# Performance work log

Hardware: AMD Instinct MI355X
Metric: run time of the kernel (lower is better)

## Reference

```python
import jax, jax.numpy as jnp
import numpy as np
import math

D, H, DK, DFF, B, T, K = 512, 8, 64, 2048, 8, 512, 31
P = 2 * T - 1  # rel-pos length


def _ln(x, g, b, eps=1e-5):
    mu = jnp.mean(x, -1, keepdims=True)
    var = jnp.var(x, -1, keepdims=True)
    return (x - mu) * jax.lax.rsqrt(var + eps) * g + b


def _silu(x):
    return x * jax.nn.sigmoid(x)


def _rel_shift(x):
    # x: [B,H,T,P] -> NeMo-style relative shift
    b, h, t, p = x.shape
    x = jnp.pad(x, ((0, 0), (0, 0), (0, 0), (1, 0)))
    x = x.reshape(b, h, p + 1, t)
    return x[:, :, 1:, :].reshape(b, h, t, p)


def _forward(x, pos_emb, ln1_g, ln1_b, ff1_w1, ff1_b1, ff1_w2, ff1_b2,
             lna_g, lna_b, wq, bq, wk, bk, wv, bv, wo, bo, wpos, pbu, pbv,
             lnc_g, lnc_b, pw1_w, pw1_b, dw_w, dw_b, cln_g, cln_b, pw2_w, pw2_b,
             ln2_g, ln2_b, ff2_w1, ff2_b1, ff2_w2, ff2_b2, lno_g, lno_b):
    b, t, d = x.shape
    h, dk = pbu.shape
    # FF1 (half-step residual)
    r = x
    y = _ln(x, ln1_g, ln1_b)
    y = _silu(y @ ff1_w1 + ff1_b1) @ ff1_w2 + ff1_b2
    r = r + 0.5 * y
    # Rel-pos multi-head attention
    y = _ln(r, lna_g, lna_b)
    q = (y @ wq + bq).reshape(b, t, h, dk)
    k = (y @ wk + bk).reshape(b, t, h, dk)
    v = (y @ wv + bv).reshape(b, t, h, dk)
    p = (pos_emb @ wpos).reshape(pos_emb.shape[0], -1, h, dk)[0]  # [P,H,dk]
    ac = jnp.einsum('bthd,bshd->bhts', q + pbu, k)
    bd = jnp.einsum('bthd,phd->bhtp', q + pbv, p)
    bd = _rel_shift(bd)[..., :t]
    attn = jax.nn.softmax((ac + bd) / math.sqrt(dk), axis=-1)
    o = jnp.einsum('bhts,bshd->bthd', attn, v).reshape(b, t, d) @ wo + bo
    r = r + o
    # Conformer convolution module (layer_norm variant)
    y = _ln(r, lnc_g, lnc_b)
    y = y @ pw1_w + pw1_b                       # [B,T,2D] pointwise conv1
    a, g = jnp.split(y, 2, axis=-1)
    y = a * jax.nn.sigmoid(g)                   # GLU over channels
    y = jnp.transpose(y, (0, 2, 1))             # [B,D,T]
    pad = (dw_w.shape[1] - 1) // 2
    y = jax.lax.conv_general_dilated(
        y, dw_w[:, None, :], (1,), [(pad, pad)],
        feature_group_count=d, dimension_numbers=('NCH', 'OIH', 'NCH'))
    y = y + dw_b[None, :, None]
    y = jnp.transpose(y, (0, 2, 1))             # [B,T,D]
    y = _ln(y, cln_g, cln_b)
    y = _silu(y) @ pw2_w + pw2_b                # pointwise conv2
    r = r + y
    # FF2 (half-step residual)
    y = _ln(r, ln2_g, ln2_b)
    y = _silu(y @ ff2_w1 + ff2_b1) @ ff2_w2 + ff2_b2
    r = r + 0.5 * y
    return _ln(r, lno_g, lno_b)


def setup_inputs() -> dict:
    key = jax.random.key(0)
    ks = iter(jax.random.split(key, 64))
    rn = lambda shape, s=0.05: jax.random.normal(next(ks), shape, dtype=jnp.float32) * s
    ones = lambda n: jnp.ones((n,), jnp.float32)
    zeros = lambda n: jnp.zeros((n,), jnp.float32)
    return dict(
        x=jax.random.normal(next(ks), (B, T, D), jnp.float32),
        pos_emb=jax.random.normal(next(ks), (1, P, D), jnp.float32),
        ln1_g=ones(D), ln1_b=zeros(D),
        ff1_w1=rn((D, DFF)), ff1_b1=zeros(DFF), ff1_w2=rn((DFF, D)), ff1_b2=zeros(D),
        lna_g=ones(D), lna_b=zeros(D),
        wq=rn((D, D)), bq=zeros(D), wk=rn((D, D)), bk=zeros(D),
        wv=rn((D, D)), bv=zeros(D), wo=rn((D, D)), bo=zeros(D),
        wpos=rn((D, D)), pbu=rn((H, DK)), pbv=rn((H, DK)),
        lnc_g=ones(D), lnc_b=zeros(D),
        pw1_w=rn((D, 2 * D)), pw1_b=zeros(2 * D),
        dw_w=rn((D, K)), dw_b=zeros(D),
        cln_g=ones(D), cln_b=zeros(D),
        pw2_w=rn((D, D)), pw2_b=zeros(D),
        ln2_g=ones(D), ln2_b=zeros(D),
        ff2_w1=rn((D, DFF)), ff2_b1=zeros(DFF), ff2_w2=rn((DFF, D)), ff2_b2=zeros(D),
        lno_g=ones(D), lno_b=zeros(D))


def reference(x, pos_emb, ln1_g, ln1_b, ff1_w1, ff1_b1, ff1_w2, ff1_b2,
              lna_g, lna_b, wq, bq, wk, bk, wv, bv, wo, bo, wpos, pbu, pbv,
              lnc_g, lnc_b, pw1_w, pw1_b, dw_w, dw_b, cln_g, cln_b, pw2_w, pw2_b,
              ln2_g, ln2_b, ff2_w1, ff2_b1, ff2_w2, ff2_b2, lno_g, lno_b):
    return _forward(x, pos_emb, ln1_g, ln1_b, ff1_w1, ff1_b1, ff1_w2, ff1_b2,
                    lna_g, lna_b, wq, bq, wk, bk, wv, bv, wo, bo, wpos, pbu, pbv,
                    lnc_g, lnc_b, pw1_w, pw1_b, dw_w, dw_b, cln_g, cln_b, pw2_w, pw2_b,
                    ln2_g, ln2_b, ff2_w1, ff2_b1, ff2_w2, ff2_b2, lno_g, lno_b)
```

## Files before the change

### kernel.cpp

```cpp
#include <hip/hip_runtime.h>
#include <hip/hip_bf16.h>

#define Bb 8
#define Tt 512
#define Dd 512
#define Hh 8
#define DKk 64
#define DFFf 2048
#define Pp 1023
#define KCc 31
#define BTt 4096
#define QS 1536

typedef __hip_bfloat16 bf16;
typedef __attribute__((ext_vector_type(8))) short short8;
typedef __attribute__((ext_vector_type(4))) short s4v;
typedef __attribute__((ext_vector_type(4))) float f32x4;

union BFU { __hip_bfloat16 h; short s; };
static __device__ __forceinline__ short bfbits(float f) {
    BFU u; u.h = __float2bfloat16(f); return u.s;
}
static __device__ __forceinline__ float bff(short s) {
    BFU u; u.s = s; return __bfloat162float(u.h);
}
static __device__ __forceinline__ unsigned pk2(float a, float b) {
    return (unsigned)(unsigned short)bfbits(a) | ((unsigned)(unsigned short)bfbits(b) << 16);
}

static __device__ __forceinline__ int dflag(const void* lg) {
    return ((const unsigned*)lg)[0] == 0x3F803F80u;
}

#define GLD16(g, l) __builtin_amdgcn_global_load_lds(                          \
    (const __attribute__((address_space(1))) void*)(g),                        \
    (__attribute__((address_space(3))) void*)(l), 16, 0, 0)

struct CvtDesc { const void* src; unsigned n; unsigned off; unsigned startBlk; };
struct CvtArgs { CvtDesc d[32]; };

__global__ __launch_bounds__(256) void cvt_batch_k(CvtArgs args, int ncv,
                                                   bf16* __restrict__ dst,
                                                   const void* __restrict__ lg) {
    int bid = blockIdx.x;
    int ti = 0;
    while (ti + 1 < ncv && bid >= (int)args.d[ti + 1].startBlk) ti++;
    CvtDesc de = args.d[ti];
    unsigned i = (bid - de.startBlk) * 256u + threadIdx.x;
    if (i >= de.n) return;
    float v;
    if (dflag(lg)) v = __bfloat162float(((const bf16*)de.src)[i]);
    else           v = ((const float*)de.src)[i];
    dst[de.off + i] = __float2bfloat16(v);
}

struct TD { const void* src; unsigned doff, R, C, startBlk; };
struct TArgs { TD d[11]; };

__global__ __launch_bounds__(256) void transpose_batch_k(TArgs ta, bf16* __restrict__ wt,
                                                         const void* __restrict__ lg) {
    int bid = blockIdx.x;
    int ti = 0;
    while (ti + 1 < 11 && bid >= (int)ta.d[ti + 1].startBlk) ti++;
    TD t = ta.d[ti];
    int tile = bid - t.startBlk;
    int ntc = t.C >> 5;
    int tr = tile / ntc, tc = tile % ntc;
    __shared__ short tl[32][33];
    short* out = (short*)wt + t.doff;
    int tx = threadIdx.x & 31, ty = threadIdx.x >> 5;
    int fl = dflag(lg);
#pragma unroll
    for (int i = 0; i < 32; i += 8) {
        size_t idx = (size_t)(tr * 32 + ty + i) * t.C + tc * 32 + tx;
        short v;
        if (fl) v = ((const short*)t.src)[idx];
        else    v = bfbits(((const float*)t.src)[idx]);
        tl[ty + i][tx] = v;
    }
    __syncthreads();
#pragma unroll
    for (int i = 0; i < 32; i += 8)
        out[(size_t)(tc * 32 + ty + i) * t.R + tr * 32 + tx] = tl[tx][ty + i];
}

__global__ __launch_bounds__(256) void prep_misc_k(const void* __restrict__ dww, bf16* __restrict__ dwT,
                                                   const void* __restrict__ bq, const void* __restrict__ bk,
                                                   const void* __restrict__ bv, bf16* __restrict__ bqkv,
                                                   const void* __restrict__ lg) {
    int i = blockIdx.x * 256 + threadIdx.x;
    int fl = dflag(lg);
    if (i < Dd * KCc) {
        int d = i / KCc, j = i % KCc;
        short v = fl ? ((const short*)dww)[i] : bfbits(((const float*)dww)[i]);
        ((short*)dwT)[j * Dd + d] = v;
    } else {
        int j = i - Dd * KCc;
        if (j < QS) {
            const void* s = (j < 512) ? bq : ((j < 1024) ? bk : bv);
            int idx = j & 511;
            short v = fl ? ((const short*)s)[idx] : bfbits(((const float*)s)[idx]);
            ((short*)bqkv)[j] = v;
        }
    }
}

template <int SILU>
__global__ __launch_bounds__(256) void ln_k(const float* __restrict__ in,
                                            const bf16* __restrict__ g,
                                            const bf16* __restrict__ b,
                                            bf16* __restrict__ out) {
    int row = blockIdx.x;
    int tid = threadIdx.x;
    float2 v = ((const float2*)(in + (size_t)row * Dd))[tid];
    float s = v.x + v.y;
    float ss = v.x * v.x + v.y * v.y;
#pragma unroll
    for (int off = 32; off > 0; off >>= 1) {
        s += __shfl_xor(s, off);
        ss += __shfl_xor(ss, off);
    }
    __shared__ float red[2][4];
    int wid = tid >> 6;
    if ((tid & 63) == 0) { red[0][wid] = s; red[1][wid] = ss; }
    __syncthreads();
    float S = red[0][0] + red[0][1] + red[0][2] + red[0][3];
    float SS = red[1][0] + red[1][1] + red[1][2] + red[1][3];
    float mean = S * (1.0f / Dd);
    float var = SS * (1.0f / Dd) - mean * mean;
    float rstd = rsqrtf(var + 1e-5f);
    unsigned gp = *(const unsigned*)((const short*)g + 2 * tid);
    unsigned bp = *(const unsigned*)((const short*)b + 2 * tid);
    float o0 = (v.x - mean) * rstd * bff((short)(gp & 0xFFFF)) + bff((short)(bp & 0xFFFF));
    float o1 = (v.y - mean) * rstd * bff((short)(gp >> 16)) + bff((short)(bp >> 16));
    if (SILU) {
        o0 = o0 / (1.0f + __expf(-o0));
        o1 = o1 / (1.0f + __expf(-o1));
    }
    *(unsigned*)((short*)out + (size_t)row * Dd + 2 * tid) = pk2(o0, o1);
}

__global__ __launch_bounds__(256) void ln_x_k(const void* __restrict__ x,
                                              const bf16* __restrict__ g,
                                              const bf16* __restrict__ b,
                                              float* __restrict__ r,
                                              bf16* __restrict__ out,
                                              const void* __restrict__ lg) {
    int row = blockIdx.x;
    int tid = threadIdx.x;
    size_t base = (size_t)row * Dd;
    float v0, v1;
    if (dflag(lg)) {
        unsigned xp = *(const unsigned*)((const short*)x + base + 2 * tid);
        v0 = bff((short)(xp & 0xFFFF));
        v1 = bff((short)(xp >> 16));
    } else {
        float2 xv = ((const float2*)((const float*)x + base))[tid];
        v0 = xv.x; v1 = xv.y;
    }
    ((float2*)(r + base))[tid] = make_float2(v0, v1);
    float s = v0 + v1;
    float ss = v0 * v0 + v1 * v1;
#pragma unroll
    for (int off = 32; off > 0; off >>= 1) {
        s += __shfl_xor(s, off);
        ss += __shfl_xor(ss, off);
    }
    __shared__ float red[2][4];
    int wid = tid >> 6;
    if ((tid & 63) == 0) { red[0][wid] = s; red[1][wid] = ss; }
    __syncthreads();
    float S = red[0][0] + red[0][1] + red[0][2] + red[0][3];
    float SS = red[1][0] + red[1][1] + red[1][2] + red[1][3];
    float mean = S * (1.0f / Dd);
    float var = SS * (1.0f / Dd) - mean * mean;
    float rstd = rsqrtf(var + 1e-5f);
    unsigned gp = *(const unsigned*)((const short*)g + 2 * tid);
    unsigned bp = *(const unsigned*)((const short*)b + 2 * tid);
    float o0 = (v0 - mean) * rstd * bff((short)(gp & 0xFFFF)) + bff((short)(bp & 0xFFFF));
    float o1 = (v1 - mean) * rstd * bff((short)(gp >> 16)) + bff((short)(bp >> 16));
    *(unsigned*)((short*)out + base + 2 * tid) = pk2(o0, o1);
}

__global__ __launch_bounds__(256) void ln_out_k(const float* __restrict__ in,
                                                const bf16* __restrict__ g,
                                                const bf16* __restrict__ b,
                                                void* __restrict__ out,
                                                const void* __restrict__ lg) {
    int row = blockIdx.x;
    int tid = threadIdx.x;
    size_t base = (size_t)row * Dd;
    float2 v = ((const float2*)(in + base))[tid];
    float s = v.x + v.y;
    float ss = v.x * v.x + v.y * v.y;
#pragma unroll
    for (int off = 32; off > 0; off >>= 1) {
        s += __shfl_xor(s, off);
        ss += __shfl_xor(ss, off);
    }
    __shared__ float red[2][4];
    int wid = tid >> 6;
    if ((tid & 63) == 0) { red[0][wid] = s; red[1][wid] = ss; }
    __syncthreads();
    float S = red[0][0] + red[0][1] + red[0][2] + red[0][3];
    float SS = red[1][0] + red[1][1] + red[1][2] + red[1][3];
    float mean = S * (1.0f / Dd);
    float var = SS * (1.0f / Dd) - mean * mean;
    float rstd = rsqrtf(var + 1e-5f);
    unsigned gp = *(const unsigned*)((const short*)g + 2 * tid);
    unsigned bp = *(const unsigned*)((const short*)b + 2 * tid);
    float o0 = (v.x - mean) * rstd * bff((short)(gp & 0xFFFF)) + bff((short)(bp & 0xFFFF));
    float o1 = (v.y - mean) * rstd * bff((short)(gp >> 16)) + bff((short)(bp >> 16));
    if (dflag(lg)) {
        *(unsigned*)((short*)out + base + 2 * tid) = pk2(o0, o1);
    } else {
        ((float2*)((float*)out + base))[tid] = make_float2(o0, o1);
    }
}

template <int BM, int BN, int BK, int WM, int WN, typename CT, int ACT, int RES, int VT>
__global__ __launch_bounds__(256) void gemm_mfma_k(const bf16* __restrict__ Abf,
                                                   const bf16* __restrict__ WT,
                                                   const bf16* __restrict__ bias,
                                                   const float* __restrict__ resid,
                                                   CT* __restrict__ C,
                                                   bf16* __restrict__ vt,
                                                   int M, int N, int Kd, float alpha) {
    constexpr int MT = WM / 16, NT = WN / 16;
    constexpr int WX = BN / WN;
    constexpr int CPB = BK / 8;
    constexpr int KS = BK / 32;
    __shared__ __align__(16) short As[BM * BK];
    __shared__ __align__(16) short Bs[BN * BK];
    int tid = threadIdx.x;
    int wid = tid >> 6, lane = tid & 63;
    int lm = lane & 15, quad = lane >> 4;
    int wy = wid / WX, wx = wid % WX;
    int bm = blockIdx.y * BM, bn = blockIdx.x * BN;
    const short* Ag = (const short*)Abf;
    const short* Bg = (const short*)WT;

    f32x4 acc[MT][NT] = {};

    for (int k0 = 0; k0 < Kd; k0 += BK) {
#pragma unroll
        for (int it = 0; it < BM * CPB / 256; it++) {
            int c = it * 256 + tid;
            int row = c / CPB;
            int q = (c % CPB) ^ (row & 7);
            int gr = bm + row;
            if (gr > M - 1) gr = M - 1;
            GLD16(Ag + (size_t)gr * Kd + k0 + q * 8, As + (it * 256 + wid * 64) * 8);
        }
#pragma unroll
        for (int it = 0; it < BN * CPB / 256; it++) {
            int c = it * 256 + tid;
            int row = c / CPB;
            int q = (c % CPB) ^ (row & 7);
            GLD16(Bg + (size_t)(bn + row) * Kd + k0 + q * 8, Bs + (it * 256 + wid * 64) * 8);
        }
        __syncthreads();
        short8 af[MT][KS], bfv[NT][KS];
#pragma unroll
        for (int mt = 0; mt < MT; mt++) {
            int row = wy * WM + mt * 16 + lm;
#pragma unroll
            for (int ks = 0; ks < KS; ks++)
                af[mt][ks] = *(const short8*)&As[row * BK + (((ks * 4 + quad) ^ (row & 7)) * 8)];
        }
#pragma unroll
        for (int nt = 0; nt < NT; nt++) {
            int row = wx * WN + nt * 16 + lm;
#pragma unroll
            for (int ks = 0; ks < KS; ks++)
                bfv[nt][ks] = *(const short8*)&Bs[row * BK + (((ks * 4 + quad) ^ (row & 7)) * 8)];
        }
#pragma unroll
        for (int ks = 0; ks < KS; ks++)
#pragma unroll
            for (int mt = 0; mt < MT; mt++)
#pragma unroll
                for (int nt = 0; nt < NT; nt++)
                    acc[mt][nt] = __builtin_amdgcn_mfma_f32_16x16x32_bf16(af[mt][ks], bfv[nt][ks], acc[mt][nt], 0, 0, 0);
        __syncthreads();
    }

#pragma unroll
    for (int mt = 0; mt < MT; mt++) {
#pragma unroll
        for (int nt = 0; nt < NT; nt++) {
            int gcol = bn + wx * WN + nt * 16 + lm;
            int growb = bm + wy * WM + mt * 16 + quad * 4;
            if (VT && gcol >= 1024) {
                float bi = bias ? __bfloat162float(bias[gcol]) : 0.f;
                s4v pk;
#pragma unroll
                for (int r = 0; r < 4; r++) pk[r] = bfbits(acc[mt][nt][r] + bi);
                *(s4v*)((short*)vt + (size_t)((growb >> 9) * 512 + (gcol - 1024)) * 512 + (growb & 511)) = pk;
            } else {
#pragma unroll
                for (int r = 0; r < 4; r++) {
                    int grow = growb + r;
                    if (grow >= M) continue;
                    float v = acc[mt][nt][r];
                    if (bias) v += __bfloat162float(bias[gcol]);
                    if (ACT == 1) v = v / (1.0f + __expf(-v));
                    if (RES == 1) v = resid[(size_t)grow * N + gcol] + alpha * v;
                    C[(size_t)grow * N + gcol] = (CT)v;
                }
            }
        }
    }
}

__global__ __launch_bounds__(256) void gemm_glu_k(const bf16* __restrict__ Abf,
                                                  const bf16* __restrict__ WT,
                                                  const bf16* __restrict__ bias,
                                                  bf16* __restrict__ C) {
    constexpr int BM = 64, BN = 64, BK = 64, WM = 32, WN = 32;
    constexpr int MT = WM / 16, NT = WN / 16, WX = BN / WN, CPB = BK / 8, KS = BK / 32;
    __shared__ __align__(16) short As[BM * BK];
    __shared__ __align__(16) short Bs[2 * BN * BK];
    int tid = threadIdx.x;
    int wid = tid >> 6, lane = tid & 63;
    int lm = lane & 15, quad = lane >> 4;
    int wy = wid / WX, wx = wid % WX;
    int bm = blockIdx.y * BM, bn = blockIdx.x * BN;
    const short* Ag = (const short*)Abf;
    const short* Bg = (const short*)WT;

    f32x4 acc[MT][NT][2] = {};

    for (int k0 = 0; k0 < Dd; k0 += BK) {
#pragma unroll
        for (int it = 0; it < BM * CPB / 256; it++) {
            int c = it * 256 + tid;
            int row = c / CPB;
            int q = (c % CPB) ^ (row & 7);
            GLD16(Ag + (size_t)(bm + row) * Dd + k0 + q * 8, As + (it * 256 + wid * 64) * 8);
        }
#pragma unroll
        for (int it = 0; it < 2 * BN * CPB / 256; it++) {
            int c = it * 256 + tid;
            int row = c / CPB;
            int q = (c % CPB) ^ (row & 7);
            int wrow = (row < BN) ? (bn + row) : (512 + bn + row - BN);
            GLD16(Bg + (size_t)wrow * Dd + k0 + q * 8, Bs + (it * 256 + wid * 64) * 8);
        }
        __syncthreads();
        short8 af[MT][KS], bfv[NT][2][KS];
#pragma unroll
        for (int mt = 0; mt < MT; mt++) {
            int row = wy * WM + mt * 16 + lm;
#pragma unroll
            for (int ks = 0; ks < KS; ks++)
                af[mt][ks] = *(const short8*)&As[row * BK + (((ks * 4 + quad) ^ (row & 7)) * 8)];
        }
#pragma unroll
        for (int nt = 0; nt < NT; nt++) {
#pragma unroll
            for (int hf = 0; hf < 2; hf++) {
                int row = hf * BN + wx * WN + nt * 16 + lm;
#pragma unroll
                for (int ks = 0; ks < KS; ks++)
                    bfv[nt][hf][ks] = *(const short8*)&Bs[row * BK + (((ks * 4 + quad) ^ (row & 7)) * 8)];
            }
        }
#pragma unroll
        for (int ks = 0; ks < KS; ks++)
#pragma unroll
            for (int mt = 0; mt < MT; mt++)
#pragma unroll
                for (int nt = 0; nt < NT; nt++) {
                    acc[mt][nt][0] = __builtin_amdgcn_mfma_f32_16x16x32_bf16(af[mt][ks], bfv[nt][0][ks], acc[mt][nt][0], 0, 0, 0);
                    acc[mt][nt][1] = __builtin_amdgcn_mfma_f32_16x16x32_bf16(af[mt][ks], bfv[nt][1][ks], acc[mt][nt][1], 0, 0, 0);
                }
        __syncthreads();
    }

#pragma unroll
    for (int mt = 0; mt < MT; mt++) {
#pragma unroll
        for (int nt = 0; nt < NT; nt++) {
#pragma unroll
            for (int r = 0; r < 4; r++) {
                int grow = bm + wy * WM + mt * 16 + quad * 4 + r;
                int gcol = bn + wx * WN + nt * 16 + lm;
                float va = acc[mt][nt][0][r] + __bfloat162float(bias[gcol]);
                float vg = acc[mt][nt][1][r] + __bfloat162float(bias[512 + gcol]);
                float v = va / (1.0f + __expf(-vg));
                C[(size_t)grow * Dd + gcol] = __float2bfloat16(v);
            }
        }
    }
}

#define SST 516

__global__ __launch_bounds__(256, 4) void attn_mfma_k(const bf16* __restrict__ qkv,
                                                      const bf16* __restrict__ p,
                                                      const bf16* __restrict__ vT,
                                                      const bf16* __restrict__ pbu,
                                                      const bf16* __restrict__ pbv,
                                                      bf16* __restrict__ out) {
    __shared__ float S[16][SST];
    __shared__ float lsum[16];
    short* Pbase = (short*)&S[0][0];
    int tid = threadIdx.x;
    int wid = tid >> 6;
    int lane = tid & 63;
    int lm = lane & 15;
    int quad = lane >> 4;
    int bidx = blockIdx.x;
    int b = bidx >> 8;
    int h = (bidx >> 5) & 7;
    int t0 = (bidx & 31) * 16;

    const short* qkvs = (const short*)qkv;
    const short* ps = (const short*)p;

    short8 qu[2], qv[2];
    {
        size_t rowbase = ((size_t)(b * Tt + t0 + lm) * QS) + h * DKk;
#pragma unroll
        for (int ksp = 0; ksp < 2; ksp++) {
            int kk = ksp * 32 + quad * 8;
            short8 raw = *(const short8*)(qkvs + rowbase + kk);
#pragma unroll
            for (int j = 0; j < 8; j++) {
                float qf = bff(raw[j]);
                qu[ksp][j] = bfbits(qf + __bfloat162float(pbu[h * DKk + kk + j]));
                qv[ksp][j] = bfbits(qf + __bfloat162float(pbv[h * DKk + kk + j]));
            }
        }
    }

    const float scale = 0.125f;

#pragma unroll
    for (int i = 0; i < 8; i++) {
        int st = wid + i * 4;
        f32x4 c = {0.f, 0.f, 0.f, 0.f};
        size_t krow = ((size_t)(b * Tt + st * 16 + lm) * QS) + 512 + h * DKk;
#pragma unroll
        for (int ksp = 0; ksp < 2; ksp++) {
            short8 bf = *(const short8*)(qkvs + krow + ksp * 32 + quad * 8);
            c = __builtin_amdgcn_mfma_f32_16x16x32_bf16(qu[ksp], bf, c, 0, 0, 0);
        }
#pragma unroll
        for (int r = 0; r < 4; r++)
            S[quad * 4 + r][st * 16 + lm] = scale * c[r];
    }
    __syncthreads();

    int win0 = 496 - t0;
#pragma unroll
    for (int i = 0; i < 8; i++) {
        int pt = wid + i * 4;
        f32x4 c = {0.f, 0.f, 0.f, 0.f};
        int prow = win0 + pt * 16 + lm;
        bool ok = (prow < Pp);
        size_t pbase = (size_t)prow * Dd + h * DKk;
#pragma unroll
        for (int ksp = 0; ksp < 2; ksp++) {
            short8 bf;
            if (ok) bf = *(const short8*)(ps + pbase + ksp * 32 + quad * 8);
            else { bf = short8{0,0,0,0,0,0,0,0}; }
            c = __builtin_amdgcn_mfma_f32_16x16x32_bf16(qv[ksp], bf, c, 0, 0, 0);
        }
#pragma unroll
        for (int r = 0; r < 4; r++) {
            int m = quad * 4 + r;
            int s = pt * 16 + lm + m - 15;
            if (s >= 0 && s < Tt) S[m][s] += scale * c[r];
        }
    }
    if (wid == 0) {
        int pt = 32;
        f32x4 c = {0.f, 0.f, 0.f, 0.f};
        int prow = win0 + pt * 16 + lm;
        bool ok = (prow < Pp);
        size_t pbase = (size_t)prow * Dd + h * DKk;
#pragma unroll
        for (int ksp = 0; ksp < 2; ksp++) {
            short8 bf;
            if (ok) bf = *(const short8*)(ps + pbase + ksp * 32 + quad * 8);
            else { bf = short8{0,0,0,0,0,0,0,0}; }
            c = __builtin_amdgcn_mfma_f32_16x16x32_bf16(qv[ksp], bf, c, 0, 0, 0);
        }
#pragma unroll
        for (int r = 0; r < 4; r++) {
            int m = quad * 4 + r;
            int s = pt * 16 + lm + m - 15;
            if (s >= 0 && s < Tt) S[m][s] += scale * c[r];
        }
    }
    __syncthreads();

    {
        int srow = tid >> 4;
        int g2 = (tid & 15) * 2;
        float mx = -1e30f;
#pragma unroll 8
        for (int i = 0; i < 16; i++) {
            mx = fmaxf(mx, fmaxf(S[srow][i * 32 + g2], S[srow][i * 32 + g2 + 1]));
        }
#pragma unroll
        for (int off = 1; off < 16; off <<= 1) mx = fmaxf(mx, __shfl_xor(mx, off));
        float sum = 0.f;
        short* prow = Pbase + (size_t)srow * (SST * 2);
#pragma unroll 8
        for (int i = 0; i < 16; i++) {
            float e0 = __expf(S[srow][i * 32 + g2] - mx);
            float e1 = __expf(S[srow][i * 32 + g2 + 1] - mx);
            sum += e0 + e1;
            *(unsigned*)&prow[i * 32 + g2] = pk2(e0, e1);
        }
#pragma unroll
        for (int off = 1; off < 16; off <<= 1) sum += __shfl_xor(sum, off);
        if (g2 == 0) lsum[srow] = sum;
    }
    __syncthreads();

    int d0 = wid * 16;
    f32x4 o = {0.f, 0.f, 0.f, 0.f};
    const short* vrow = (const short*)vT + ((size_t)(b * Hh + h) * DKk + d0 + lm) * Tt;
    const short* parow = Pbase + (size_t)lm * (SST * 2);
#pragma unroll
    for (int ksp = 0; ksp < 16; ksp++) {
        int kk = ksp * 32 + quad * 8;
        short8 a = *(const short8*)(parow + kk);
        short8 bf = *(const short8*)(vrow + kk);
        o = __builtin_amdgcn_mfma_f32_16x16x32_bf16(a, bf, o, 0, 0, 0);
    }
    short* os = (short*)out;
#pragma unroll
    for (int r = 0; r < 4; r++) {
        int m = quad * 4 + r;
        os[((size_t)(b * Tt + t0 + m) * Dd) + h * DKk + d0 + lm] = bfbits(o[r] / lsum[m]);
    }
}

__global__ __launch_bounds__(256) void dwconv_ln_k(const bf16* __restrict__ in,
                                                   const bf16* __restrict__ wT,
                                                   const bf16* __restrict__ bdw,
                                                   const bf16* __restrict__ g,
                                                   const bf16* __restrict__ bb,
                                                   bf16* __restrict__ out) {
    int row = blockIdx.x * 4 + (threadIdx.x >> 6);
    int lane = threadIdx.x & 63;
    int d0 = lane * 8;
    int t = row & 511, b = row >> 9;
    const short* ins = (const short*)in + (size_t)b * Tt * Dd;
    const short* wts = (const short*)wT;
    float acc[8];
    short8 bv = *(const short8*)((const short*)bdw + d0);
#pragma unroll
    for (int e = 0; e < 8; e++) acc[e] = bff(bv[e]);
#pragma unroll
    for (int j = 0; j < KCc; j++) {
        int tt = t + j - 15;
        if (tt < 0 || tt >= Tt) continue;
        short8 iv = *(const short8*)(ins + (size_t)tt * Dd + d0);
        short8 wv = *(const short8*)(wts + j * Dd + d0);
#pragma unroll
        for (int e = 0; e < 8; e++) acc[e] += bff(iv[e]) * bff(wv[e]);
    }
    float s = 0.f, ss = 0.f;
#pragma unroll
    for (int e = 0; e < 8; e++) { s += acc[e]; ss += acc[e] * acc[e]; }
#pragma unroll
    for (int off = 32; off > 0; off >>= 1) {
        s += __shfl_xor(s, off);
        ss += __shfl_xor(ss, off);
    }
    float mean = s * (1.0f / Dd);
    float var = ss * (1.0f / Dd) - mean * mean;
    float rstd = rsqrtf(var + 1e-5f);
    short8 gv = *(const short8*)((const short*)g + d0);
    short8 bbv = *(const short8*)((const short*)bb + d0);
    short8 ov;
#pragma unroll
    for (int e = 0; e < 8; e++) {
        float o = (acc[e] - mean) * rstd * bff(gv[e]) + bff(bbv[e]);
        o = o / (1.0f + __expf(-o));
        ov[e] = bfbits(o);
    }
    *(short8*)((short*)out + (size_t)row * Dd + d0) = ov;
}

extern "C" void kernel_launch(void* const* d_in, const int* in_sizes, int n_in,
                              void* d_out, int out_size, void* d_ws, size_t ws_size,
                              hipStream_t stream) {
    char* base = (char*)d_ws;
    bf16* wb = (bf16*)(base + 256);

    size_t woff[39];
    size_t acc = 0;
    for (int i = 1; i < 39; i++) { woff[i] = acc; acc += (size_t)in_sizes[i]; }
    size_t wbytes = (2 * acc + 255) & ~(size_t)255;

    const size_t NBT = (size_t)BTt * Dd;
    float* r   = (float*)((char*)wb + wbytes);
    bf16* a    = (bf16*)((char*)r + NBT * 4);
    bf16* big  = a + NBT;
    bf16* pbuf = big + (size_t)BTt * DFFf;
    bf16* wt   = pbuf + (size_t)Pp * Dd;

    const void* lg = d_in[2];

    bf16* c_pos   = wb + woff[1];
    bf16* c_ln1g  = wb + woff[2],  *c_ln1b = wb + woff[3];
    bf16* c_f1b1  = wb + woff[5];
    bf16* c_f1b2  = wb + woff[7];
    bf16* c_lnag  = wb + woff[8],  *c_lnab = wb + woff[9];
    bf16* c_bo    = wb + woff[17];
    bf16* c_pbu   = wb + woff[19], *c_pbv  = wb + woff[20];
    bf16* c_lncg  = wb + woff[21], *c_lncb = wb + woff[22];
    bf16* c_p1b   = wb + woff[24];
    bf16* c_dwb   = wb + woff[26];
    bf16* c_clng  = wb + woff[27], *c_clnb = wb + woff[28];
    bf16* c_p2b   = wb + woff[30];
    bf16* c_ln2g  = wb + woff[31], *c_ln2b = wb + woff[32];
    bf16* c_f2b1  = wb + woff[34];
    bf16* c_f2b2  = wb + woff[36];
    bf16* c_lnog  = wb + woff[37], *c_lnob = wb + woff[38];

    const int tin[11]  = {4, 6, 10, 12, 14, 16, 18, 23, 29, 33, 35};
    const unsigned tR[11] = {512, 2048, 512, 512, 512, 512, 512, 512, 512, 512, 2048};
    const unsigned tC[11] = {2048, 512, 512, 512, 512, 512, 512, 1024, 512, 2048, 512};
    size_t toff[11]; size_t tacc = 0;
    for (int i = 0; i < 11; i++) { toff[i] = tacc; tacc += (size_t)tR[i] * tC[i]; }
    bf16* t_f1w1 = wt + toff[0];
    bf16* t_f1w2 = wt + toff[1];
    bf16* t_wqkv = wt + toff[2];
    bf16* t_wo   = wt + toff[5];
    bf16* t_wpos = wt + toff[6];
    bf16* t_p1w  = wt + toff[7];
    bf16* t_p2w  = wt + toff[8];
    bf16* t_f2w1 = wt + toff[9];
    bf16* t_f2w2 = wt + toff[10];
    bf16* bias_qkv = wt + tacc;
    bf16* dwT      = bias_qkv + QS;
    bf16* vTb      = dwT + KCc * Dd;

    dim3 blk(256);

    bool skip[39] = {};
    for (int i = 0; i < 11; i++) skip[tin[i]] = true;
    skip[11] = skip[13] = skip[15] = skip[25] = true;
    CvtArgs ca;
    int ncv = 0;
    unsigned blkacc = 0;
    for (int i = 1; i < 39; i++) {
        if (skip[i]) continue;
        ca.d[ncv].src = d_in[i];
        ca.d[ncv].n = (unsigned)in_sizes[i];
        ca.d[ncv].off = (unsigned)woff[i];
        ca.d[ncv].startBlk = blkacc;
        blkacc += (unsigned)((in_sizes[i] + 255) / 256);
        ncv++;
    }
    cvt_batch_k<<<blkacc, blk, 0, stream>>>(ca, ncv, wb, lg);

    TArgs ta;
    unsigned tblk = 0;
    for (int i = 0; i < 11; i++) {
        ta.d[i].src = d_in[tin[i]];
        ta.d[i].doff = (unsigned)toff[i];
        ta.d[i].R = tR[i];
        ta.d[i].C = tC[i];
        ta.d[i].startBlk = tblk;
        tblk += (tR[i] >> 5) * (tC[i] >> 5);
    }
    transpose_batch_k<<<tblk, blk, 0, stream>>>(ta, wt, lg);
    prep_misc_k<<<(Dd * KCc + QS + 255) / 256, blk, 0, stream>>>(
        d_in[25], dwT, d_in[11], d_in[13], d_in[15], bias_qkv, lg);

    auto g128 = [](int M, int N) { return dim3(N / 128, M / 128); };
    auto g64  = [](int M, int N) { return dim3(N / 64, (M + 63) / 64); };

    ln_x_k<<<BTt, blk, 0, stream>>>(d_in[0], c_ln1g, c_ln1b, r, a, lg);
    gemm_mfma_k<128, 128, 64, 64, 64, bf16, 1, 0, 0><<<g128(BTt, DFFf), blk, 0, stream>>>(
        a, t_f1w1, c_f1b1, nullptr, big, nullptr, BTt, DFFf, Dd, 0.f);
    gemm_mfma_k<64, 64, 128, 32, 32, float, 0, 1, 0><<<g64(BTt, Dd), blk, 0, stream>>>(
        big, t_f1w2, c_f1b2, r, r, nullptr, BTt, Dd, DFFf, 0.5f);

    bf16* qkvb = big;
    bf16* cb   = big + 3 * NBT;
    ln_k<0><<<BTt, blk, 0, stream>>>(r, c_lnag, c_lnab, a);
    gemm_mfma_k<128, 64, 64, 64, 32, bf16, 0, 0, 1><<<dim3(QS / 64, BTt / 128), blk, 0, stream>>>(
        a, t_wqkv, bias_qkv, nullptr, qkvb, vTb, BTt, QS, Dd, 0.f);
    gemm_mfma_k<64, 64, 64, 32, 32, bf16, 0, 0, 0><<<g64(Pp, Dd), blk, 0, stream>>>(
        c_pos, t_wpos, nullptr, nullptr, pbuf, nullptr, Pp, Dd, Dd, 0.f);
    attn_mfma_k<<<Bb * Hh * (Tt / 16), blk, 0, stream>>>(qkvb, pbuf, vTb, c_pbu, c_pbv, cb);
    gemm_mfma_k<64, 64, 64, 32, 32, float, 0, 1, 0><<<g64(BTt, Dd), blk, 0, stream>>>(
        cb, t_wo, c_bo, r, r, nullptr, BTt, Dd, Dd, 1.0f);

    bf16* gluo = big + 2 * NBT;
    ln_k<0><<<BTt, blk, 0, stream>>>(r, c_lncg, c_lncb, a);
    gemm_glu_k<<<dim3(Dd / 64, BTt / 64), blk, 0, stream>>>(a, t_p1w, c_p1b, gluo);
    dwconv_ln_k<<<BTt / 4, blk, 0, stream>>>(gluo, dwT, c_dwb, c_clng, c_clnb, a);
    gemm_mfma_k<64, 64, 64, 32, 32, float, 0, 1, 0><<<g64(BTt, Dd), blk, 0, stream>>>(
        a, t_p2w, c_p2b, r, r, nullptr, BTt, Dd, Dd, 1.0f);

    ln_k<0><<<BTt, blk, 0, stream>>>(r, c_ln2g, c_ln2b, a);
    gemm_mfma_k<128, 128, 64, 64, 64, bf16, 1, 0, 0><<<g128(BTt, DFFf), blk, 0, stream>>>(
        a, t_f2w1, c_f2b1, nullptr, big, nullptr, BTt, DFFf, Dd, 0.f);
    gemm_mfma_k<64, 64, 128, 32, 32, float, 0, 1, 0><<<g64(BTt, Dd), blk, 0, stream>>>(
        big, t_f2w2, c_f2b2, r, r, nullptr, BTt, Dd, DFFf, 0.5f);

    ln_out_k<<<BTt, blk, 0, stream>>>(r, c_lnog, c_lnob, d_out, lg);
}
```

Before: 433.1 us.

## Fuse content and positional score tiles with shuffle-based relative shift

```diff
diff --git a/kernel.cpp b/kernel.cpp
--- a/kernel.cpp
+++ b/kernel.cpp
@@ -422,97 +422,86 @@
     short8 qu[2], qv[2];
     {
         size_t rowbase = ((size_t)(b * Tt + t0 + lm) * QS) + h * DKk;
+        const short* pbus = (const short*)pbu + h * DKk + quad * 8;
+        const short* pbvs = (const short*)pbv + h * DKk + quad * 8;
 #pragma unroll
         for (int ksp = 0; ksp < 2; ksp++) {
-            int kk = ksp * 32 + quad * 8;
-            short8 raw = *(const short8*)(qkvs + rowbase + kk);
+            short8 raw = *(const short8*)(qkvs + rowbase + ksp * 32 + quad * 8);
+            short8 bu = *(const short8*)(pbus + ksp * 32);
+            short8 bv = *(const short8*)(pbvs + ksp * 32);
 #pragma unroll
             for (int j = 0; j < 8; j++) {
                 float qf = bff(raw[j]);
-                qu[ksp][j] = bfbits(qf + __bfloat162float(pbu[h * DKk + kk + j]));
-                qv[ksp][j] = bfbits(qf + __bfloat162float(pbv[h * DKk + kk + j]));
+                qu[ksp][j] = bfbits(qf + bff(bu[j]));
+                qv[ksp][j] = bfbits(qf + bff(bv[j]));
             }
         }
     }
 
     const float scale = 0.125f;
 
+    int pb0 = 511 - t0 + wid * 128;
+
+    f32x4 dprev = {0.f, 0.f, 0.f, 0.f};
+    {
+        int prow = pb0 - 16 + lm;
+        if (prow < 0) prow = 0;
+        size_t pa = (size_t)prow * Dd + h * DKk;
+#pragma unroll
+        for (int ksp = 0; ksp < 2; ksp++) {
+            short8 pf = *(const short8*)(ps + pa + ksp * 32 + quad * 8);
+            dprev = __builtin_amdgcn_mfma_f32_16x16x32_bf16(qv[ksp], pf, dprev, 0, 0, 0);
+        }
+    }
+
 #pragma unroll
     for (int i = 0; i < 8; i++) {
-        int st = wid + i * 4;
-        f32x4 c = {0.f, 0.f, 0.f, 0.f};
+        int st = wid * 8 + i;
+        f32x4 ac = {0.f, 0.f, 0.f, 0.f};
+        f32x4 dcur = {0.f, 0.f, 0.f, 0.f};
         size_t krow = ((size_t)(b * Tt + st * 16 + lm) * QS) + 512 + h * DKk;
+        size_t pa = (size_t)(pb0 + i * 16 + lm) * Dd + h * DKk;
 #pragma unroll
         for (int ksp = 0; ksp < 2; ksp++) {
-            short8 bf = *(const short8*)(qkvs + krow + ksp * 32 + quad * 8);
-            c = __builtin_amdgcn_mfma_f32_16x16x32_bf16(qu[ksp], bf, c, 0, 0, 0);
-        }
-#pragma unroll
-        for (int r = 0; r < 4; r++)
-            S[quad * 4 + r][st * 16 + lm] = scale * c[r];
-    }
-    __syncthreads();
-
-    int win0 = 496 - t0;
-#pragma unroll
-    for (int i = 0; i < 8; i++) {
-        int pt = wid + i * 4;
-        f32x4 c = {0.f, 0.f, 0.f, 0.f};
-        int prow = win0 + pt * 16 + lm;
-        bool ok = (prow < Pp);
-        size_t pbase = (size_t)prow * Dd + h * DKk;
-#pragma unroll
-        for (int ksp = 0; ksp < 2; ksp++) {
-            short8 bf;
-            if (ok) bf = *(const short8*)(ps + pbase + ksp * 32 + quad * 8);
-            else { bf = short8{0,0,0,0,0,0,0,0}; }
-            c = __builtin_amdgcn_mfma_f32_16x16x32_bf16(qv[ksp], bf, c, 0, 0, 0);
+            short8 kf = *(const short8*)(qkvs + krow + ksp * 32 + quad * 8);
+            short8 pf = *(const short8*)(ps + pa + ksp * 32 + quad * 8);
+            ac = __builtin_amdgcn_mfma_f32_16x16x32_bf16(qu[ksp], kf, ac, 0, 0, 0);
+            dcur = __builtin_amdgcn_mfma_f32_16x16x32_bf16(qv[ksp], pf, dcur, 0, 0, 0);
         }
 #pragma unroll
         for (int r = 0; r < 4; r++) {
             int m = quad * 4 + r;
-            int s = pt * 16 + lm + m - 15;
-            if (s >= 0 && s < Tt) S[m][s] += scale * c[r];
-        }
-    }
-    if (wid == 0) {
-        int pt = 32;
-        f32x4 c = {0.f, 0.f, 0.f, 0.f};
-        int prow = win0 + pt * 16 + lm;
-        bool ok = (prow < Pp);
-        size_t pbase = (size_t)prow * Dd + h * DKk;
-#pragma unroll
-        for (int ksp = 0; ksp < 2; ksp++) {
-            short8 bf;
-            if (ok) bf = *(const short8*)(ps + pbase + ksp * 32 + quad * 8);
-            else { bf = short8{0,0,0,0,0,0,0,0}; }
-            c = __builtin_amdgcn_mfma_f32_16x16x32_bf16(qv[ksp], bf, c, 0, 0, 0);
-        }
-#pragma unroll
-        for (int r = 0; r < 4; r++) {
-            int m = quad * 4 + r;
-            int s = pt * 16 + lm + m - 15;
-            if (s >= 0 && s < Tt) S[m][s] += scale * c[r];
-        }
+            int j = (lm - m) & 15;
+            int srcl = quad * 16 + j;
+            float b2 = __shfl(dcur[r], srcl, 64);
+            float b1 = __shfl(dprev[r], srcl, 64);
+            float bd = (lm >= m) ? b2 : b1;
+            S[m][st * 16 + lm] = scale * (ac[r] + bd);
+        }
+        dprev = dcur;
     }
     __syncthreads();
 
     {
         int srow = tid >> 4;
         int g2 = (tid & 15) * 2;
+        float vals[32];
         float mx = -1e30f;
-#pragma unroll 8
+#pragma unroll
         for (int i = 0; i < 16; i++) {
-            mx = fmaxf(mx, fmaxf(S[srow][i * 32 + g2], S[srow][i * 32 + g2 + 1]));
+            float2 v = *(const float2*)&S[srow][i * 32 + g2];
+            vals[2 * i] = v.x;
+            vals[2 * i + 1] = v.y;
+            mx = fmaxf(mx, fmaxf(v.x, v.y));
         }
 #pragma unroll
         for (int off = 1; off < 16; off <<= 1) mx = fmaxf(mx, __shfl_xor(mx, off));
         float sum = 0.f;
         short* prow = Pbase + (size_t)srow * (SST * 2);
-#pragma unroll 8
+#pragma unroll
         for (int i = 0; i < 16; i++) {
-            float e0 = __expf(S[srow][i * 32 + g2] - mx);
-            float e1 = __expf(S[srow][i * 32 + g2 + 1] - mx);
+            float e0 = __expf(vals[2 * i] - mx);
+            float e1 = __expf(vals[2 * i + 1] - mx);
             sum += e0 + e1;
             *(unsigned*)&prow[i * 32 + g2] = pk2(e0, e1);
         }
```

After: 439.4 us. About the same (+1.5%).
